# Performance work log

Measured on AMD Instinct MI355X. Metric: run time of the kernel, lower is better.

Reference implementation:

```python
import jax, jax.numpy as jnp
import numpy as np

NF4 = jnp.array([-1.0, -0.6961928009986877, -0.5250730514526367, -0.39491748809814453,
                 -0.28444138169288635, -0.18477343022823334, -0.09105003625154495, 0.0,
                 0.07958029955625534, 0.16093020141124725, 0.24611230850219726,
                 0.33791524171829224, 0.44070982933044434, 0.5626170039176941,
                 0.7229568362236023, 1.0], dtype=jnp.float32)

OUT, IN = 8192, 8192
BLOCK = 64
NUMEL = OUT * IN


def setup_inputs() -> dict:
    key = jax.random.key(0)
    k1, k2, k3, k4 = jax.random.split(key, 4)
    x = jax.random.normal(k1, (64, IN), dtype=jnp.float32)
    packed = jax.random.randint(k2, (NUMEL // 2,), 0, 256, dtype=jnp.int32)
    absmax = jax.random.uniform(k3, (NUMEL // BLOCK,), dtype=jnp.float32)
    bias = jax.random.normal(k4, (OUT,), dtype=jnp.float32)
    return {"x": x, "packed": packed, "absmax": absmax, "bias": bias}


def nf4_dequantize(packed, absmax):
    # packed holds two 4-bit codes per byte: low nibble first, then high nibble
    low = packed & 15
    high = (packed >> 4) & 15
    q = jnp.stack([low, high], axis=1).reshape(-1)          # [numel]
    normalized = NF4[q]                                      # LUT dequant
    groups = normalized.reshape(-1, BLOCK)                   # [numel/block, block]
    w = (groups * absmax[:, None]).reshape(-1)[:NUMEL]
    return w.reshape(OUT, IN)


def reference(x, packed, absmax, bias):
    w = nf4_dequantize(packed, absmax)                       # [out, in]
    return jnp.dot(x, w.T) + bias                            # F.linear
```

## Files before the change

### kernel.cpp

```cpp
#include <hip/hip_runtime.h>
#include <hip/hip_bf16.h>

#define OUT_N 8192
#define IN_K  8192
#define M_ROWS 64

typedef __attribute__((ext_vector_type(8))) short  bf16x8;
typedef __attribute__((ext_vector_type(4))) float  f32x4;
typedef __attribute__((ext_vector_type(4))) int    int4v;
typedef __attribute__((ext_vector_type(2))) int    int2v;

__device__ const float NF4_TAB[16] = {
  -1.0f, -0.6961928009986877f, -0.5250730514526367f, -0.39491748809814453f,
  -0.28444138169288635f, -0.18477343022823334f, -0.09105003625154495f, 0.0f,
  0.07958029955625534f, 0.16093020141124725f, 0.24611230850219726f,
  0.33791524171829224f, 0.44070982933044434f, 0.5626170039176941f,
  0.7229568362236023f, 1.0f };

static __device__ __forceinline__ unsigned short f2bf(float f) {
  union { __hip_bfloat16 h; unsigned short s; } u;
  u.h = __float2bfloat16(f);
  return u.s;
}

static __device__ __forceinline__ void gload_lds16(const void* g, void* s) {
  __builtin_amdgcn_global_load_lds((const __attribute__((address_space(1))) void*)g,
                                   (__attribute__((address_space(3))) void*)s,
                                   16, 0, 0);
}

__global__ __launch_bounds__(256) void qlin_prep(const float* __restrict__ x,
                                                 unsigned short* __restrict__ xf) {
  int t = blockIdx.x * 256 + threadIdx.x;
  int lane = t & 63, mt = (t >> 6) & 3, ks = t >> 8;
  int ri = lane & 15, kbb = lane >> 4;
  const float* src = x + (size_t)(mt * 16 + ri) * IN_K + ks * 32 + kbb * 8;
  f32x4 a = *(const f32x4*)src;
  f32x4 c = *(const f32x4*)(src + 4);
  bf16x8 o;
  o[0] = (short)f2bf(a[0]); o[1] = (short)f2bf(a[1]);
  o[2] = (short)f2bf(a[2]); o[3] = (short)f2bf(a[3]);
  o[4] = (short)f2bf(c[0]); o[5] = (short)f2bf(c[1]);
  o[6] = (short)f2bf(c[2]); o[7] = (short)f2bf(c[3]);
  ((bf16x8*)xf)[t] = o;
}

static __device__ __forceinline__ bf16x8 deq(const unsigned int* lut, unsigned b) {
  int4v bw;
  bw[0] = (int)lut[b & 255];
  bw[1] = (int)lut[(b >> 8) & 255];
  bw[2] = (int)lut[(b >> 16) & 255];
  bw[3] = (int)lut[b >> 24];
  union { int4v i; bf16x8 h; } c; c.i = bw;
  return c.h;
}

#define STAGE(BUF, PH) {                                                      \
    const char* _s = xfb + (((size_t)(PH) * 4 + w) * 4096) + l * 16;          \
    gload_lds16(_s,        &ast[BUF][w][0]);                                  \
    gload_lds16(_s + 1024, &ast[BUF][w][64]);                                 \
    gload_lds16(_s + 2048, &ast[BUF][w][128]);                                \
    gload_lds16(_s + 3072, &ast[BUF][w][192]); }

#define CSTEP_BODY(S, PKV)                                                    \
    int _nk = KS + (S) + 4; if (_nk > NITm1) _nk = NITm1;                     \
    int4v _npk = *(const int4v*)(pcoal + (size_t)_nk * 64);                   \
    bf16x8 A0 = ast[cur][S][l];                                               \
    bf16x8 A1 = ast[cur][S][64 + l];                                          \
    bf16x8 A2 = ast[cur][S][128 + l];                                         \
    bf16x8 A3 = ast[cur][S][192 + l];                                         \
    unsigned _pkd = (unsigned)PKV[0] | ((unsigned)PKV[1] << 8)                \
                  | ((unsigned)PKV[2] << 16) | ((unsigned)PKV[3] << 24);      \
    unsigned _bp = (unsigned)__builtin_amdgcn_ds_bpermute(bpidx, (int)_pkd);  \
    bf16x8 b = deq(lut, _bp);

#define CSTEP_EVEN(S, PKV) {                                                  \
    CSTEP_BODY(S, PKV)                                                        \
    sb0 = __builtin_amdgcn_mfma_f32_16x16x32_bf16(A0, b, zro, 0, 0, 0);       \
    sb1 = __builtin_amdgcn_mfma_f32_16x16x32_bf16(A1, b, zro, 0, 0, 0);       \
    sb2 = __builtin_amdgcn_mfma_f32_16x16x32_bf16(A2, b, zro, 0, 0, 0);       \
    sb3 = __builtin_amdgcn_mfma_f32_16x16x32_bf16(A3, b, zro, 0, 0, 0);       \
    PKV = _npk; }

#define CSTEP_ODD(S, PKV, AM) {                                               \
    CSTEP_BODY(S, PKV)                                                        \
    sb0 = __builtin_amdgcn_mfma_f32_16x16x32_bf16(A0, b, sb0, 0, 0, 0);       \
    sb1 = __builtin_amdgcn_mfma_f32_16x16x32_bf16(A1, b, sb1, 0, 0, 0);       \
    sb2 = __builtin_amdgcn_mfma_f32_16x16x32_bf16(A2, b, sb2, 0, 0, 0);       \
    sb3 = __builtin_amdgcn_mfma_f32_16x16x32_bf16(A3, b, sb3, 0, 0, 0);       \
    mn0 += sb0 * (AM); mn1 += sb1 * (AM);                                     \
    mn2 += sb2 * (AM); mn3 += sb3 * (AM);                                     \
    PKV = _npk; }

template<int NC>
__global__ __launch_bounds__(256, 4) void qlin_main(
    const int*   __restrict__ packed,
    const float* __restrict__ absmax,
    const unsigned short* __restrict__ xf,
    unsigned short* __restrict__ parts) {
  constexpr int KCn   = IN_K / NC;
  constexpr int NIT   = KCn / 32;
  constexpr int NITm1 = NIT - 1;
  constexpr int NPH   = NIT / 4;
  constexpr int AMX   = NIT / 2 - 1;
  constexpr int LOG   = (NC == 8) ? 3 : 2;

  __shared__ unsigned int lut[256];
  __shared__ bf16x8 ast[2][4][256];
  {
    int t = threadIdx.x;
    unsigned lo = f2bf(NF4_TAB[t & 15]);
    unsigned hi = f2bf(NF4_TAB[(t >> 4) & 15]);
    lut[t] = lo | (hi << 16);
  }
  __syncthreads();

  const int l     = threadIdx.x & 63;
  const int w     = threadIdx.x >> 6;
  const int ntile = (int)blockIdx.x >> LOG;
  const int chunk = (int)blockIdx.x & (NC - 1);
  const int colg0 = ntile * 64 + w * 16;
  const int col   = colg0 + (l & 15);
  const int kb    = l >> 4;
  const int kc0   = chunk * KCn;
  const int ksg0  = kc0 >> 5;

  const char* pcoal = (const char*)packed
                    + ((size_t)(colg0 + (l >> 2)) * (IN_K / 2) + kc0 / 2) * 4
                    + (l & 3) * 16;
  const int bpidx = (((l & 15) << 2) | (l >> 4)) << 2;

  const char* xfb = (const char*)xf + (size_t)ksg0 * 4096;
  const float* aptr = absmax + (size_t)col * 128 + (kc0 >> 6);

  const f32x4 zro = {0.f, 0.f, 0.f, 0.f};
  f32x4 mn0 = zro, mn1 = zro, mn2 = zro, mn3 = zro;
  f32x4 sb0, sb1, sb2, sb3;
  int4v pk0, pk1, pk2, pk3;

  float amE = aptr[0], amO = aptr[1];
  STAGE(0, 0);
  __builtin_amdgcn_sched_barrier(0);
  pk0 = *(const int4v*)(pcoal);
  pk1 = *(const int4v*)(pcoal + 64);
  pk2 = *(const int4v*)(pcoal + 128);
  pk3 = *(const int4v*)(pcoal + 192);
  asm volatile("s_waitcnt vmcnt(4)" ::: "memory");
  __builtin_amdgcn_s_barrier();

  for (int ph = 0; ph < NPH; ++ph) {
    const int KS  = ph * 4;
    const int cur = ph & 1;

    int ia = 2 * ph + 2; if (ia > AMX) ia = AMX;
    int ib = 2 * ph + 3; if (ib > AMX) ib = AMX;
    float pmE = aptr[ia], pmO = aptr[ib];
    if (ph + 1 < NPH) STAGE(cur ^ 1, ph + 1);
    __builtin_amdgcn_sched_barrier(0);

    CSTEP_EVEN(0, pk0)
    CSTEP_ODD (1, pk1, amE)
    CSTEP_EVEN(2, pk2)
    CSTEP_ODD (3, pk3, amO)

    amE = pmE; amO = pmO;
    asm volatile("s_waitcnt vmcnt(4)" ::: "memory");
    asm volatile("s_waitcnt lgkmcnt(0)" ::: "memory");
    __builtin_amdgcn_s_barrier();
  }

  {
    float* tl = (float*)&ast[0][0][0];
    const int c  = w * 16 + (l & 15);
    const int r0 = kb * 4;
    tl[(0  + r0 + 0) * 68 + c] = mn0[0];
    tl[(0  + r0 + 1) * 68 + c] = mn0[1];
    tl[(0  + r0 + 2) * 68 + c] = mn0[2];
    tl[(0  + r0 + 3) * 68 + c] = mn0[3];
    tl[(16 + r0 + 0) * 68 + c] = mn1[0];
    tl[(16 + r0 + 1) * 68 + c] = mn1[1];
    tl[(16 + r0 + 2) * 68 + c] = mn1[2];
    tl[(16 + r0 + 3) * 68 + c] = mn1[3];
    tl[(32 + r0 + 0) * 68 + c] = mn2[0];
    tl[(32 + r0 + 1) * 68 + c] = mn2[1];
    tl[(32 + r0 + 2) * 68 + c] = mn2[2];
    tl[(32 + r0 + 3) * 68 + c] = mn2[3];
    tl[(48 + r0 + 0) * 68 + c] = mn3[0];
    tl[(48 + r0 + 1) * 68 + c] = mn3[1];
    tl[(48 + r0 + 2) * 68 + c] = mn3[2];
    tl[(48 + r0 + 3) * 68 + c] = mn3[3];
    __syncthreads();
    unsigned short* po = parts + ((size_t)chunk * 128 + ntile) * 4096;
    const int t  = threadIdx.x;
    const int rr = t >> 4;
    const int cq = (t & 15) * 4;
    #pragma unroll
    for (int p = 0; p < 4; ++p) {
      const int row = p * 16 + rr;
      f32x4 v = *(const f32x4*)&tl[row * 68 + cq];
      int2v o;
      o[0] = (int)(f2bf(v[0]) | ((unsigned)f2bf(v[1]) << 16));
      o[1] = (int)(f2bf(v[2]) | ((unsigned)f2bf(v[3]) << 16));
      *(int2v*)(po + (size_t)row * 64 + cq) = o;
    }
  }
}

template<int NC>
__global__ __launch_bounds__(256) void qlin_reduce(
    const unsigned short* __restrict__ parts,
    const float* __restrict__ bias,
    float*       __restrict__ out) {
  int e = blockIdx.x * 256 + threadIdx.x;
  if (e >= M_ROWS * OUT_N / 8) return;
  const int tile = e >> 9;
  const int rem  = e & 511;
  const int row  = rem >> 3;
  const int oct  = rem & 7;
  const size_t base = ((size_t)tile * 64 + row) * 64 + oct * 8;
  constexpr size_t CS = (size_t)128 * 64 * 64;
  float s[8] = {0,0,0,0,0,0,0,0};
  #pragma unroll
  for (int c = 0; c < NC; ++c) {
    bf16x8 v = *(const bf16x8*)(parts + c * CS + base);
    #pragma unroll
    for (int j = 0; j < 8; ++j)
      s[j] += __uint_as_float(((unsigned)(unsigned short)v[j]) << 16);
  }
  const int colb = tile * 64 + oct * 8;
  const f32x4* bp = (const f32x4*)(bias + colb);
  f32x4 b0 = bp[0], b1 = bp[1];
  f32x4 o0, o1;
  o0[0] = s[0] + b0[0]; o0[1] = s[1] + b0[1];
  o0[2] = s[2] + b0[2]; o0[3] = s[3] + b0[3];
  o1[0] = s[4] + b1[0]; o1[1] = s[5] + b1[1];
  o1[2] = s[6] + b1[2]; o1[3] = s[7] + b1[3];
  float* op = out + (size_t)row * OUT_N + colb;
  *(f32x4*)op = o0;
  *(f32x4*)(op + 4) = o1;
}

extern "C" void kernel_launch(void* const* d_in, const int* in_sizes, int n_in,
                              void* d_out, int out_size, void* d_ws, size_t ws_size,
                              hipStream_t stream) {
  const float* x      = (const float*)d_in[0];
  const int*   packed = (const int*)d_in[1];
  const float* absmax = (const float*)d_in[2];
  const float* bias   = (const float*)d_in[3];
  float* out = (float*)d_out;

  unsigned short* xf    = (unsigned short*)d_ws;
  unsigned short* parts = (unsigned short*)((char*)d_ws + (1 << 20));

  qlin_prep<<<(M_ROWS * IN_K / 8 + 255) / 256, 256, 0, stream>>>(x, xf);

  const size_t chunk_bytes = (size_t)128 * 64 * 64 * sizeof(unsigned short);
  const size_t need8 = (size_t)(1 << 20) + 8 * chunk_bytes;
  if (ws_size >= need8) {
    qlin_main<8><<<128 * 8, 256, 0, stream>>>(packed, absmax, xf, parts);
    qlin_reduce<8><<<(M_ROWS * OUT_N / 8 + 255) / 256, 256, 0, stream>>>(parts, bias, out);
  } else {
    qlin_main<4><<<128 * 4, 256, 0, stream>>>(packed, absmax, xf, parts);
    qlin_reduce<4><<<(M_ROWS * OUT_N / 8 + 255) / 256, 256, 0, stream>>>(parts, bias, out);
  }
}
```

Measured before the change: 38.83 us.

## Load activations directly into registers and fold absmax scale into dequant

Drops the LDS double-buffered staging of activations (global_load_lds plus per-phase barriers) and instead has each wave load its bf16 A fragments straight from global memory into registers, prefetching one step ahead. The absmax scaling moves out of the fp32 accumulator path into the dequantization: each weight is scaled in fp32 and rounded to bf16 before the MFMA, so the kernel accumulates directly instead of using separate partial sums. This removes barriers and the extra vector multiply-adds, but adds per-element conversion work and redundant global reads of activations across the four waves. It also rounds the scaled weight to bf16, which changes numerics slightly.

```diff
diff --git a/kernel.cpp b/kernel.cpp
--- a/kernel.cpp
+++ b/kernel.cpp
@@ -21,12 +21,6 @@
   union { __hip_bfloat16 h; unsigned short s; } u;
   u.h = __float2bfloat16(f);
   return u.s;
-}
-
-static __device__ __forceinline__ void gload_lds16(const void* g, void* s) {
-  __builtin_amdgcn_global_load_lds((const __attribute__((address_space(1))) void*)g,
-                                   (__attribute__((address_space(3))) void*)s,
-                                   16, 0, 0);
 }
 
 __global__ __launch_bounds__(256) void qlin_prep(const float* __restrict__ x,
@@ -45,52 +39,42 @@
   ((bf16x8*)xf)[t] = o;
 }
 
-static __device__ __forceinline__ bf16x8 deq(const unsigned int* lut, unsigned b) {
-  int4v bw;
-  bw[0] = (int)lut[b & 255];
-  bw[1] = (int)lut[(b >> 8) & 255];
-  bw[2] = (int)lut[(b >> 16) & 255];
-  bw[3] = (int)lut[b >> 24];
-  union { int4v i; bf16x8 h; } c; c.i = bw;
-  return c.h;
-}
-
-#define STAGE(BUF, PH) {                                                      \
-    const char* _s = xfb + (((size_t)(PH) * 4 + w) * 4096) + l * 16;          \
-    gload_lds16(_s,        &ast[BUF][w][0]);                                  \
-    gload_lds16(_s + 1024, &ast[BUF][w][64]);                                 \
-    gload_lds16(_s + 2048, &ast[BUF][w][128]);                                \
-    gload_lds16(_s + 3072, &ast[BUF][w][192]); }
-
-#define CSTEP_BODY(S, PKV)                                                    \
-    int _nk = KS + (S) + 4; if (_nk > NITm1) _nk = NITm1;                     \
-    int4v _npk = *(const int4v*)(pcoal + (size_t)_nk * 64);                   \
-    bf16x8 A0 = ast[cur][S][l];                                               \
-    bf16x8 A1 = ast[cur][S][64 + l];                                          \
-    bf16x8 A2 = ast[cur][S][128 + l];                                         \
-    bf16x8 A3 = ast[cur][S][192 + l];                                         \
+static __device__ __forceinline__ bf16x8 deqscale(const unsigned int* lut,
+                                                  unsigned b, float am) {
+  unsigned p0 = lut[b & 255];
+  unsigned p1 = lut[(b >> 8) & 255];
+  unsigned p2 = lut[(b >> 16) & 255];
+  unsigned p3 = lut[b >> 24];
+  bf16x8 r;
+  r[0] = (short)f2bf(__uint_as_float(p0 << 16) * am);
+  r[1] = (short)f2bf(__uint_as_float(p0 & 0xffff0000u) * am);
+  r[2] = (short)f2bf(__uint_as_float(p1 << 16) * am);
+  r[3] = (short)f2bf(__uint_as_float(p1 & 0xffff0000u) * am);
+  r[4] = (short)f2bf(__uint_as_float(p2 << 16) * am);
+  r[5] = (short)f2bf(__uint_as_float(p2 & 0xffff0000u) * am);
+  r[6] = (short)f2bf(__uint_as_float(p3 << 16) * am);
+  r[7] = (short)f2bf(__uint_as_float(p3 & 0xffff0000u) * am);
+  return r;
+}
+
+#define QSTEP(U4, PKV, AMV) {                                                 \
+    int aks = KS + (U4) + 1; if (aks > NITm1) aks = NITm1;                    \
+    int pks = KS + (U4) + 4; if (pks > NITm1) pks = NITm1;                    \
+    const char* _ap = xbase + (size_t)aks * 4096;                             \
+    bf16x8 n0 = *(const bf16x8*)(_ap);                                        \
+    bf16x8 n1 = *(const bf16x8*)(_ap + 1024);                                 \
+    bf16x8 n2 = *(const bf16x8*)(_ap + 2048);                                 \
+    bf16x8 n3 = *(const bf16x8*)(_ap + 3072);                                 \
+    int4v npk = *(const int4v*)(pcoal + (size_t)pks * 64);                    \
     unsigned _pkd = (unsigned)PKV[0] | ((unsigned)PKV[1] << 8)                \
                   | ((unsigned)PKV[2] << 16) | ((unsigned)PKV[3] << 24);      \
     unsigned _bp = (unsigned)__builtin_amdgcn_ds_bpermute(bpidx, (int)_pkd);  \
-    bf16x8 b = deq(lut, _bp);
-
-#define CSTEP_EVEN(S, PKV) {                                                  \
-    CSTEP_BODY(S, PKV)                                                        \
-    sb0 = __builtin_amdgcn_mfma_f32_16x16x32_bf16(A0, b, zro, 0, 0, 0);       \
-    sb1 = __builtin_amdgcn_mfma_f32_16x16x32_bf16(A1, b, zro, 0, 0, 0);       \
-    sb2 = __builtin_amdgcn_mfma_f32_16x16x32_bf16(A2, b, zro, 0, 0, 0);       \
-    sb3 = __builtin_amdgcn_mfma_f32_16x16x32_bf16(A3, b, zro, 0, 0, 0);       \
-    PKV = _npk; }
-
-#define CSTEP_ODD(S, PKV, AM) {                                               \
-    CSTEP_BODY(S, PKV)                                                        \
-    sb0 = __builtin_amdgcn_mfma_f32_16x16x32_bf16(A0, b, sb0, 0, 0, 0);       \
-    sb1 = __builtin_amdgcn_mfma_f32_16x16x32_bf16(A1, b, sb1, 0, 0, 0);       \
-    sb2 = __builtin_amdgcn_mfma_f32_16x16x32_bf16(A2, b, sb2, 0, 0, 0);       \
-    sb3 = __builtin_amdgcn_mfma_f32_16x16x32_bf16(A3, b, sb3, 0, 0, 0);       \
-    mn0 += sb0 * (AM); mn1 += sb1 * (AM);                                     \
-    mn2 += sb2 * (AM); mn3 += sb3 * (AM);                                     \
-    PKV = _npk; }
+    bf16x8 b = deqscale(lut, _bp, AMV);                                       \
+    mn0 = __builtin_amdgcn_mfma_f32_16x16x32_bf16(A0, b, mn0, 0, 0, 0);       \
+    mn1 = __builtin_amdgcn_mfma_f32_16x16x32_bf16(A1, b, mn1, 0, 0, 0);       \
+    mn2 = __builtin_amdgcn_mfma_f32_16x16x32_bf16(A2, b, mn2, 0, 0, 0);       \
+    mn3 = __builtin_amdgcn_mfma_f32_16x16x32_bf16(A3, b, mn3, 0, 0, 0);       \
+    A0 = n0; A1 = n1; A2 = n2; A3 = n3; PKV = npk; }
 
 template<int NC>
 __global__ __launch_bounds__(256, 4) void qlin_main(
@@ -101,12 +85,12 @@
   constexpr int KCn   = IN_K / NC;
   constexpr int NIT   = KCn / 32;
   constexpr int NITm1 = NIT - 1;
-  constexpr int NPH   = NIT / 4;
+  constexpr int NGRP  = NIT / 4;
   constexpr int AMX   = NIT / 2 - 1;
   constexpr int LOG   = (NC == 8) ? 3 : 2;
 
   __shared__ unsigned int lut[256];
-  __shared__ bf16x8 ast[2][4][256];
+  __shared__ float tl[64 * 68];
   {
     int t = threadIdx.x;
     unsigned lo = f2bf(NF4_TAB[t & 15]);
@@ -130,47 +114,39 @@
                     + (l & 3) * 16;
   const int bpidx = (((l & 15) << 2) | (l >> 4)) << 2;
 
-  const char* xfb = (const char*)xf + (size_t)ksg0 * 4096;
+  const char* xbase = (const char*)xf + (size_t)ksg0 * 4096 + l * 16;
   const float* aptr = absmax + (size_t)col * 128 + (kc0 >> 6);
 
   const f32x4 zro = {0.f, 0.f, 0.f, 0.f};
   f32x4 mn0 = zro, mn1 = zro, mn2 = zro, mn3 = zro;
-  f32x4 sb0, sb1, sb2, sb3;
+  bf16x8 A0, A1, A2, A3;
   int4v pk0, pk1, pk2, pk3;
 
-  float amE = aptr[0], amO = aptr[1];
-  STAGE(0, 0);
-  __builtin_amdgcn_sched_barrier(0);
+  A0 = *(const bf16x8*)(xbase);
+  A1 = *(const bf16x8*)(xbase + 1024);
+  A2 = *(const bf16x8*)(xbase + 2048);
+  A3 = *(const bf16x8*)(xbase + 3072);
   pk0 = *(const int4v*)(pcoal);
   pk1 = *(const int4v*)(pcoal + 64);
   pk2 = *(const int4v*)(pcoal + 128);
   pk3 = *(const int4v*)(pcoal + 192);
-  asm volatile("s_waitcnt vmcnt(4)" ::: "memory");
-  __builtin_amdgcn_s_barrier();
-
-  for (int ph = 0; ph < NPH; ++ph) {
-    const int KS  = ph * 4;
-    const int cur = ph & 1;
-
-    int ia = 2 * ph + 2; if (ia > AMX) ia = AMX;
-    int ib = 2 * ph + 3; if (ib > AMX) ib = AMX;
+  float amE = aptr[0], amO = aptr[1];
+
+  for (int g = 0; g < NGRP; ++g) {
+    const int KS = g * 4;
+    int ia = 2 * g + 2; if (ia > AMX) ia = AMX;
+    int ib = 2 * g + 3; if (ib > AMX) ib = AMX;
     float pmE = aptr[ia], pmO = aptr[ib];
-    if (ph + 1 < NPH) STAGE(cur ^ 1, ph + 1);
-    __builtin_amdgcn_sched_barrier(0);
-
-    CSTEP_EVEN(0, pk0)
-    CSTEP_ODD (1, pk1, amE)
-    CSTEP_EVEN(2, pk2)
-    CSTEP_ODD (3, pk3, amO)
+
+    QSTEP(0, pk0, amE)
+    QSTEP(1, pk1, amE)
+    QSTEP(2, pk2, amO)
+    QSTEP(3, pk3, amO)
 
     amE = pmE; amO = pmO;
-    asm volatile("s_waitcnt vmcnt(4)" ::: "memory");
-    asm volatile("s_waitcnt lgkmcnt(0)" ::: "memory");
-    __builtin_amdgcn_s_barrier();
   }
 
   {
-    float* tl = (float*)&ast[0][0][0];
     const int c  = w * 16 + (l & 15);
     const int r0 = kb * 4;
     tl[(0  + r0 + 0) * 68 + c] = mn0[0];
```

Result: slower. 45.49 us (+17.2%).

## Halve LDS staging of activations, read rest from global, split K into 16 chunks

Applied to the files above, without the earlier changes.

Only the first two 16-row activation groups are staged in LDS. The other two are loaded straight from global memory (L2-resident) in each step. The epilogue converts to bf16 before writing to a union-shared LDS tile and stores 16-byte vectors. The K dimension is split into 16 chunks instead of 8, so twice as many blocks run, and the vmcnt wait is adjusted for the extra in-flight global loads. This cuts LDS footprint and raises parallelism, at the cost of more partial-sum traffic in the reduce and more global loads per step.

```diff
diff --git a/kernel.cpp b/kernel.cpp
--- a/kernel.cpp
+++ b/kernel.cpp
@@ -8,7 +8,6 @@
 typedef __attribute__((ext_vector_type(8))) short  bf16x8;
 typedef __attribute__((ext_vector_type(4))) float  f32x4;
 typedef __attribute__((ext_vector_type(4))) int    int4v;
-typedef __attribute__((ext_vector_type(2))) int    int2v;
 
 __device__ const float NF4_TAB[16] = {
   -1.0f, -0.6961928009986877f, -0.5250730514526367f, -0.39491748809814453f,
@@ -55,20 +54,27 @@
   return c.h;
 }
 
+union SMem {
+  struct {
+    unsigned int lut[256];
+    bf16x8 ast[2][4][128];
+  } s;
+  unsigned short tlb[64][72];
+};
+
 #define STAGE(BUF, PH) {                                                      \
     const char* _s = xfb + (((size_t)(PH) * 4 + w) * 4096) + l * 16;          \
     gload_lds16(_s,        &ast[BUF][w][0]);                                  \
-    gload_lds16(_s + 1024, &ast[BUF][w][64]);                                 \
-    gload_lds16(_s + 2048, &ast[BUF][w][128]);                                \
-    gload_lds16(_s + 3072, &ast[BUF][w][192]); }
+    gload_lds16(_s + 1024, &ast[BUF][w][64]); }
 
 #define CSTEP_BODY(S, PKV)                                                    \
-    int _nk = KS + (S) + 4; if (_nk > NITm1) _nk = NITm1;                     \
-    int4v _npk = *(const int4v*)(pcoal + (size_t)_nk * 64);                   \
+    int _pks = KS + (S) + 4; if (_pks > NITm1) _pks = NITm1;                  \
+    const char* _gp = xfb + (size_t)(KS + (S)) * 4096 + l * 16;               \
+    bf16x8 A2 = *(const bf16x8*)(_gp + 2048);                                 \
+    bf16x8 A3 = *(const bf16x8*)(_gp + 3072);                                 \
+    int4v _npk = *(const int4v*)(pcoal + (size_t)_pks * 64);                  \
     bf16x8 A0 = ast[cur][S][l];                                               \
     bf16x8 A1 = ast[cur][S][64 + l];                                          \
-    bf16x8 A2 = ast[cur][S][128 + l];                                         \
-    bf16x8 A3 = ast[cur][S][192 + l];                                         \
     unsigned _pkd = (unsigned)PKV[0] | ((unsigned)PKV[1] << 8)                \
                   | ((unsigned)PKV[2] << 16) | ((unsigned)PKV[3] << 24);      \
     unsigned _bp = (unsigned)__builtin_amdgcn_ds_bpermute(bpidx, (int)_pkd);  \
@@ -103,17 +109,19 @@
   constexpr int NITm1 = NIT - 1;
   constexpr int NPH   = NIT / 4;
   constexpr int AMX   = NIT / 2 - 1;
-  constexpr int LOG   = (NC == 8) ? 3 : 2;
-
-  __shared__ unsigned int lut[256];
-  __shared__ bf16x8 ast[2][4][256];
+  constexpr int LOG   = (NC == 16) ? 4 : 3;
+
+  __shared__ SMem sm;
+  auto& lutm = sm.s.lut;
+  auto& ast  = sm.s.ast;
   {
     int t = threadIdx.x;
     unsigned lo = f2bf(NF4_TAB[t & 15]);
     unsigned hi = f2bf(NF4_TAB[(t >> 4) & 15]);
-    lut[t] = lo | (hi << 16);
+    lutm[t] = lo | (hi << 16);
   }
   __syncthreads();
+  const unsigned int* lut = &lutm[0];
 
   const int l     = threadIdx.x & 63;
   const int w     = threadIdx.x >> 6;
@@ -164,44 +172,40 @@
     CSTEP_ODD (3, pk3, amO)
 
     amE = pmE; amO = pmO;
-    asm volatile("s_waitcnt vmcnt(4)" ::: "memory");
+    asm volatile("s_waitcnt vmcnt(12)" ::: "memory");
     asm volatile("s_waitcnt lgkmcnt(0)" ::: "memory");
     __builtin_amdgcn_s_barrier();
   }
 
   {
-    float* tl = (float*)&ast[0][0][0];
     const int c  = w * 16 + (l & 15);
     const int r0 = kb * 4;
-    tl[(0  + r0 + 0) * 68 + c] = mn0[0];
-    tl[(0  + r0 + 1) * 68 + c] = mn0[1];
-    tl[(0  + r0 + 2) * 68 + c] = mn0[2];
-    tl[(0  + r0 + 3) * 68 + c] = mn0[3];
-    tl[(16 + r0 + 0) * 68 + c] = mn1[0];
-    tl[(16 + r0 + 1) * 68 + c] = mn1[1];
-    tl[(16 + r0 + 2) * 68 + c] = mn1[2];
-    tl[(16 + r0 + 3) * 68 + c] = mn1[3];
-    tl[(32 + r0 + 0) * 68 + c] = mn2[0];
-    tl[(32 + r0 + 1) * 68 + c] = mn2[1];
-    tl[(32 + r0 + 2) * 68 + c] = mn2[2];
-    tl[(32 + r0 + 3) * 68 + c] = mn2[3];
-    tl[(48 + r0 + 0) * 68 + c] = mn3[0];
-    tl[(48 + r0 + 1) * 68 + c] = mn3[1];
-    tl[(48 + r0 + 2) * 68 + c] = mn3[2];
-    tl[(48 + r0 + 3) * 68 + c] = mn3[3];
+    sm.tlb[0  + r0 + 0][c] = f2bf(mn0[0]);
+    sm.tlb[0  + r0 + 1][c] = f2bf(mn0[1]);
+    sm.tlb[0  + r0 + 2][c] = f2bf(mn0[2]);
+    sm.tlb[0  + r0 + 3][c] = f2bf(mn0[3]);
+    sm.tlb[16 + r0 + 0][c] = f2bf(mn1[0]);
+    sm.tlb[16 + r0 + 1][c] = f2bf(mn1[1]);
+    sm.tlb[16 + r0 + 2][c] = f2bf(mn1[2]);
+    sm.tlb[16 + r0 + 3][c] = f2bf(mn1[3]);
+    sm.tlb[32 + r0 + 0][c] = f2bf(mn2[0]);
+    sm.tlb[32 + r0 + 1][c] = f2bf(mn2[1]);
+    sm.tlb[32 + r0 + 2][c] = f2bf(mn2[2]);
+    sm.tlb[32 + r0 + 3][c] = f2bf(mn2[3]);
+    sm.tlb[48 + r0 + 0][c] = f2bf(mn3[0]);
+    sm.tlb[48 + r0 + 1][c] = f2bf(mn3[1]);
+    sm.tlb[48 + r0 + 2][c] = f2bf(mn3[2]);
+    sm.tlb[48 + r0 + 3][c] = f2bf(mn3[3]);
     __syncthreads();
     unsigned short* po = parts + ((size_t)chunk * 128 + ntile) * 4096;
-    const int t  = threadIdx.x;
-    const int rr = t >> 4;
-    const int cq = (t & 15) * 4;
+    const int t   = threadIdx.x;
+    const int rr  = t >> 3;
+    const int oct = (t & 7) * 8;
     #pragma unroll
-    for (int p = 0; p < 4; ++p) {
-      const int row = p * 16 + rr;
-      f32x4 v = *(const f32x4*)&tl[row * 68 + cq];
-      int2v o;
-      o[0] = (int)(f2bf(v[0]) | ((unsigned)f2bf(v[1]) << 16));
-      o[1] = (int)(f2bf(v[2]) | ((unsigned)f2bf(v[3]) << 16));
-      *(int2v*)(po + (size_t)row * 64 + cq) = o;
+    for (int p = 0; p < 2; ++p) {
+      const int row = p * 32 + rr;
+      bf16x8 v = *(const bf16x8*)&sm.tlb[row][oct];
+      *(bf16x8*)(po + (size_t)row * 64 + oct) = v;
     }
   }
 }
@@ -255,12 +259,12 @@
   qlin_prep<<<(M_ROWS * IN_K / 8 + 255) / 256, 256, 0, stream>>>(x, xf);
 
   const size_t chunk_bytes = (size_t)128 * 64 * 64 * sizeof(unsigned short);
-  const size_t need8 = (size_t)(1 << 20) + 8 * chunk_bytes;
-  if (ws_size >= need8) {
+  const size_t need16 = (size_t)(1 << 20) + 16 * chunk_bytes;
+  if (ws_size >= need16) {
+    qlin_main<16><<<128 * 16, 256, 0, stream>>>(packed, absmax, xf, parts);
+    qlin_reduce<16><<<(M_ROWS * OUT_N / 8 + 255) / 256, 256, 0, stream>>>(parts, bias, out);
+  } else {
     qlin_main<8><<<128 * 8, 256, 0, stream>>>(packed, absmax, xf, parts);
     qlin_reduce<8><<<(M_ROWS * OUT_N / 8 + 255) / 256, 256, 0, stream>>>(parts, bias, out);
-  } else {
-    qlin_main<4><<<128 * 4, 256, 0, stream>>>(packed, absmax, xf, parts);
-    qlin_reduce<4><<<(M_ROWS * OUT_N / 8 + 255) / 256, 256, 0, stream>>>(parts, bias, out);
-  }
-}
+  }
+}
```

New measurement: 42.80 us. 1.1x slower.
